# Kernel tuning notes

Measured on AMD Instinct MI355X. Metric: run time of the kernel, lower is better.

The kernel has to match this reference:

```python
import jax, jax.numpy as jnp
import numpy as np

B, S, D, H = 2, 2048, 1024, 16
DK = D // H

def setup_inputs() -> dict:
    key = jax.random.key(0)
    ks = jax.random.split(key, 11)
    scale = 1.0 / np.sqrt(D)
    inp = {
        'query': jax.random.normal(ks[0], (B, S, D), jnp.float32),
        'key':   jax.random.normal(ks[1], (B, S, D), jnp.float32),
        'value': jax.random.normal(ks[2], (B, S, D), jnp.float32),
        'wq': jax.random.normal(ks[3], (D, D), jnp.float32) * scale,
        'bq': jax.random.normal(ks[4], (D,), jnp.float32) * 0.01,
        'wk': jax.random.normal(ks[5], (D, D), jnp.float32) * scale,
        'bk': jax.random.normal(ks[6], (D,), jnp.float32) * 0.01,
        'wv': jax.random.normal(ks[7], (D, D), jnp.float32) * scale,
        'bv': jax.random.normal(ks[8], (D,), jnp.float32) * 0.01,
        'wo': jax.random.normal(ks[9], (D, D), jnp.float32) * scale,
        'bo': jax.random.normal(ks[10], (D,), jnp.float32) * 0.01,
    }
    return inp

def reference(query, key, value, wq, bq, wk, bk, wv, bv, wo, bo):
    nb = query.shape[0]
    # projections: torch nn.Linear computes x @ W^T + b; here weights stored as (in,out)
    def proj(x, w, b):
        return (x @ w + b).reshape(nb, -1, H, DK).transpose(0, 2, 1, 3)  # [B,H,S,dk]
    q = proj(query, wq, bq)
    k = proj(key, wk, bk)
    v = proj(value, wv, bv)
    scores = jnp.einsum('bhqd,bhkd->bhqk', q, k) / jnp.sqrt(jnp.float32(DK))
    p = jax.nn.softmax(scores, axis=-1)  # dropout p=0 (eval)
    x = jnp.einsum('bhqk,bhkd->bhqd', p, v)
    x = x.transpose(0, 2, 1, 3).reshape(nb, -1, H * DK)
    return x @ wo + bo
```

## Files before the change

kernel.cpp:

```cpp
#include <hip/hip_runtime.h>


typedef __attribute__((ext_vector_type(8))) __bf16 bf16x8;
typedef __attribute__((ext_vector_type(4))) __bf16 bf16x4;
typedef __attribute__((ext_vector_type(8))) float f32x8;
typedef __attribute__((ext_vector_type(4))) float f32x4;

#define MFMA16 __builtin_amdgcn_mfma_f32_16x16x32_bf16

union Bf8 { bf16x8 v; __bf16 e[8]; };

__device__ inline f32x4 zero4() { f32x4 z; z[0]=z[1]=z[2]=z[3]=0.f; return z; }

__device__ inline void load_lds16(const void* g, void* l) {
    __builtin_amdgcn_global_load_lds(
        (const __attribute__((address_space(1))) unsigned int*)g,
        (__attribute__((address_space(3))) unsigned int*)l, 16, 0, 0);
}

__global__ __launch_bounds__(256) void prep_all(
        const float* __restrict__ w0, const float* __restrict__ w1,
        const float* __restrict__ w2, const float* __restrict__ w3,
        const float* __restrict__ x0, const float* __restrict__ x1,
        const float* __restrict__ x2,
        __bf16* __restrict__ wt, __bf16* __restrict__ xb) {
    const int z = blockIdx.z;
    const int t = threadIdx.x;
    if (z < 4) {
        const float* src = z == 0 ? w0 : z == 1 ? w1 : z == 2 ? w2 : w3;
        __bf16* dst = wt + (size_t)z * 1048576;
        __shared__ float tile[32][33];
        const int tc = t & 31, tr = t >> 5;
        const int r0 = blockIdx.y * 32, c0 = blockIdx.x * 32;
#pragma unroll
        for (int i = 0; i < 4; i++) {
            int r = tr + i * 8;
            tile[r][tc] = src[(size_t)(r0 + r) * 1024 + c0 + tc];
        }
        __syncthreads();
#pragma unroll
        for (int i = 0; i < 4; i++) {
            int r = tr + i * 8;
            dst[(size_t)(c0 + r) * 1024 + r0 + tc] = (__bf16)tile[tc][r];
        }
    } else {
        const float* src = z == 4 ? x0 : z == 5 ? x1 : x2;
        __bf16* dst = xb + (size_t)(z - 4) * 4194304;
        int bid = blockIdx.y * 32 + blockIdx.x;
        size_t g = ((size_t)bid * 256 + t) * 16;
#pragma unroll
        for (int h = 0; h < 2; h++) {
            f32x8 a = *(const f32x8*)&src[g + h * 8];
            Bf8 tmp;
#pragma unroll
            for (int j = 0; j < 8; j++) tmp.e[j] = (__bf16)a[j];
            *(bf16x8*)&dst[g + h * 8] = tmp.v;
        }
    }
}

template <int MODE, typename OutT>
__device__ inline void gemm_fast_core(const __bf16* __restrict__ A,
                                      const __bf16* __restrict__ Bt,
                                      const float* __restrict__ bias,
                                      OutT* __restrict__ out, float scale) {
    __shared__ __bf16 As[8192];
    __shared__ __bf16 Bs[8192];
    const int t = threadIdx.x;
    const int wave = t >> 6, lane = t & 63, lm = lane & 15, quad = lane >> 4;
    const int m0 = blockIdx.y * 128, n0 = blockIdx.x * 128;
    const int wm = (wave >> 1) * 64, wn = (wave & 1) * 64;

    f32x4 acc[4][4];
#pragma unroll
    for (int i = 0; i < 4; i++)
#pragma unroll
        for (int j = 0; j < 4; j++) acc[i][j] = zero4();

    for (int k0 = 0; k0 < 1024; k0 += 64) {
#pragma unroll
        for (int i = 0; i < 4; i++) {
            int s = i * 256 + t;
            int row = s >> 3, cb = (s & 7) ^ (row & 7);
            size_t goff = (size_t)row * 1024 + k0 + cb * 8;
            __bf16* lbase = (__bf16*)((size_t)(i * 256 + wave * 64) * 8);
            load_lds16(&A[(size_t)m0 * 1024 + goff], &As[(size_t)(i * 256 + wave * 64) * 8]);
            load_lds16(&Bt[(size_t)n0 * 1024 + goff], &Bs[(size_t)(i * 256 + wave * 64) * 8]);
            (void)lbase;
        }
        __syncthreads();
#pragma unroll
        for (int ks = 0; ks < 2; ks++) {
            bf16x8 af[4], bfr[4];
#pragma unroll
            for (int mt = 0; mt < 4; mt++)
                af[mt] = *(const bf16x8*)&As[(wm + mt * 16 + lm) * 64 +
                                             (((ks * 4 + quad) ^ (lm & 7)) * 8)];
#pragma unroll
            for (int nt = 0; nt < 4; nt++)
                bfr[nt] = *(const bf16x8*)&Bs[(wn + nt * 16 + lm) * 64 +
                                              (((ks * 4 + quad) ^ (lm & 7)) * 8)];
#pragma unroll
            for (int mt = 0; mt < 4; mt++)
#pragma unroll
                for (int nt = 0; nt < 4; nt++)
                    acc[mt][nt] = MFMA16(af[mt], bfr[nt], acc[mt][nt], 0, 0, 0);
        }
        __syncthreads();
    }

    float bv4[4];
#pragma unroll
    for (int nt = 0; nt < 4; nt++) bv4[nt] = bias[n0 + wn + nt * 16 + lm];

#pragma unroll
    for (int mt = 0; mt < 4; mt++) {
#pragma unroll
        for (int r = 0; r < 4; r++) {
            int row = m0 + wm + mt * 16 + quad * 4 + r;
#pragma unroll
            for (int nt = 0; nt < 4; nt++) {
                int col = n0 + wn + nt * 16 + lm;
                float val = (acc[mt][nt][r] + bv4[nt]) * scale;
                size_t idx;
                if (MODE == 0) {
                    idx = (size_t)row * 1024 + col;
                } else {
                    int b = row >> 11, s = row & 2047, hh = col >> 6, dk = col & 63;
                    if (MODE == 1)
                        idx = (size_t)(b * 16 + hh) * 131072 + (size_t)s * 64 + dk;
                    else
                        idx = (size_t)(b * 16 + hh) * 131072 + (size_t)dk * 2048 + s;
                }
                out[idx] = (OutT)val;
            }
        }
    }
}

__global__ __launch_bounds__(256) void proj_fast(
        const __bf16* __restrict__ Xb, const __bf16* __restrict__ WT,
        const float* __restrict__ bq, const float* __restrict__ bk,
        const float* __restrict__ bv,
        __bf16* __restrict__ Q, __bf16* __restrict__ K, __bf16* __restrict__ Vt) {
    int z = blockIdx.z;
    if (z == 0)
        gemm_fast_core<1, __bf16>(Xb, WT, bq, Q, 0.125f);
    else if (z == 1)
        gemm_fast_core<1, __bf16>(Xb + 4194304, WT + 1048576, bk, K, 1.f);
    else
        gemm_fast_core<2, __bf16>(Xb + 8388608, WT + 2097152, bv, Vt, 1.f);
}

__global__ __launch_bounds__(256) void out_proj_fast(
        const __bf16* __restrict__ A, const __bf16* __restrict__ Bt,
        const float* __restrict__ bias, float* __restrict__ out) {
    gemm_fast_core<0, float>(A, Bt, bias, out, 1.f);
}

template <int MODE>
__device__ inline void gemm_core(const float* __restrict__ A,
                                 const __bf16* __restrict__ Bt,
                                 const float* __restrict__ bias,
                                 __bf16* __restrict__ out, float scale) {
    __shared__ __bf16 As[128 * 72];
    __shared__ __bf16 Bs[128 * 72];
    const int t = threadIdx.x;
    const int wave = t >> 6, lane = t & 63, lm = lane & 15, quad = lane >> 4;
    const int m0 = blockIdx.y * 128, n0 = blockIdx.x * 128;
    const int wm = (wave >> 1) * 64, wn = (wave & 1) * 64;

    f32x4 acc[4][4];
#pragma unroll
    for (int i = 0; i < 4; i++)
#pragma unroll
        for (int j = 0; j < 4; j++) acc[i][j] = zero4();

    for (int k0 = 0; k0 < 1024; k0 += 64) {
#pragma unroll
        for (int i = 0; i < 4; i++) {
            int c = i * 256 + t;
            int row = c >> 3, c8 = c & 7;
            size_t aoff = (size_t)(m0 + row) * 1024 + k0 + c8 * 8;
            f32x8 a = *(const f32x8*)&A[aoff];
            Bf8 tmp;
#pragma unroll
            for (int j = 0; j < 8; j++) tmp.e[j] = (__bf16)a[j];
            *(bf16x8*)&As[row * 72 + c8 * 8] = tmp.v;
            *(bf16x8*)&Bs[row * 72 + c8 * 8] =
                *(const bf16x8*)&Bt[(size_t)(n0 + row) * 1024 + k0 + c8 * 8];
        }
        __syncthreads();
#pragma unroll
        for (int ks = 0; ks < 2; ks++) {
            bf16x8 af[4], bfr[4];
#pragma unroll
            for (int mt = 0; mt < 4; mt++)
                af[mt] = *(const bf16x8*)&As[(wm + mt * 16 + lm) * 72 + ks * 32 + quad * 8];
#pragma unroll
            for (int nt = 0; nt < 4; nt++)
                bfr[nt] = *(const bf16x8*)&Bs[(wn + nt * 16 + lm) * 72 + ks * 32 + quad * 8];
#pragma unroll
            for (int mt = 0; mt < 4; mt++)
#pragma unroll
                for (int nt = 0; nt < 4; nt++)
                    acc[mt][nt] = MFMA16(af[mt], bfr[nt], acc[mt][nt], 0, 0, 0);
        }
        __syncthreads();
    }

    float bv4[4];
#pragma unroll
    for (int nt = 0; nt < 4; nt++) bv4[nt] = bias[n0 + wn + nt * 16 + lm];

#pragma unroll
    for (int mt = 0; mt < 4; mt++) {
#pragma unroll
        for (int r = 0; r < 4; r++) {
            int row = m0 + wm + mt * 16 + quad * 4 + r;
#pragma unroll
            for (int nt = 0; nt < 4; nt++) {
                int col = n0 + wn + nt * 16 + lm;
                float val = (acc[mt][nt][r] + bv4[nt]) * scale;
                size_t idx;
                int b = row >> 11, s = row & 2047, hh = col >> 6, dk = col & 63;
                if (MODE == 1)
                    idx = (size_t)(b * 16 + hh) * 131072 + (size_t)s * 64 + dk;
                else
                    idx = (size_t)(b * 16 + hh) * 131072 + (size_t)dk * 2048 + s;
                out[idx] = (__bf16)val;
            }
        }
    }
}

__global__ __launch_bounds__(256) void proj_slow(
        const float* __restrict__ q, const float* __restrict__ k,
        const float* __restrict__ v, const __bf16* __restrict__ WT,
        const float* __restrict__ bq, const float* __restrict__ bk,
        const float* __restrict__ bv,
        __bf16* __restrict__ Q, __bf16* __restrict__ K, __bf16* __restrict__ Vt) {
    int z = blockIdx.z;
    if (z == 0)      gemm_core<1>(q, WT,           bq, Q,  0.125f);
    else if (z == 1) gemm_core<1>(k, WT + 1048576, bk, K,  1.f);
    else             gemm_core<2>(v, WT + 2097152, bv, Vt, 1.f);
}

__global__ __launch_bounds__(256, 2) void attn_kernel(
        const __bf16* __restrict__ Q, const __bf16* __restrict__ K,
        const __bf16* __restrict__ Vt, __bf16* __restrict__ O) {
    __shared__ __bf16 Ks[8192];
    __shared__ __bf16 Vs[8192];
    __shared__ __bf16 Ps[4 * 32 * 136];
    const int t = threadIdx.x;
    const int wave = t >> 6, lane = t & 63, lm = lane & 15, quad = lane >> 4;
    const int q0 = blockIdx.x * 128;
    const int bh = blockIdx.y;
    const size_t base = (size_t)bh * 131072;

    bf16x8 bq[2][2];
    {
        int qrow = q0 + wave * 32;
#pragma unroll
        for (int nt = 0; nt < 2; nt++)
#pragma unroll
            for (int ks = 0; ks < 2; ks++)
                bq[nt][ks] = *(const bf16x8*)
                    &Q[base + (size_t)(qrow + nt * 16 + lm) * 64 + ks * 32 + quad * 8];
    }

    float m_run[2], l_run[2];
#pragma unroll
    for (int n = 0; n < 2; n++) { m_run[n] = -1e30f; l_run[n] = 0.f; }
    f32x4 o_acc[4][2];
#pragma unroll
    for (int mt = 0; mt < 4; mt++)
#pragma unroll
        for (int n = 0; n < 2; n++) o_acc[mt][n] = zero4();

    __bf16* Pw = &Ps[wave * 32 * 136];

    for (int kv0 = 0; kv0 < 2048; kv0 += 128) {
#pragma unroll
        for (int i = 0; i < 4; i++) {
            int s = i * 256 + t;
            {
                int row = s >> 3, cb = (s & 7) ^ (row & 7);
                load_lds16(&K[base + (size_t)(kv0 + row) * 64 + cb * 8],
                           &Ks[(size_t)(i * 256 + wave * 64) * 8]);
            }
            {
                int row = s >> 4, cb = (s & 15) ^ (row & 15);
                load_lds16(&Vt[base + (size_t)row * 2048 + kv0 + cb * 8],
                           &Vs[(size_t)(i * 256 + wave * 64) * 8]);
            }
        }
        __syncthreads();

        f32x4 sc[8][2];
#pragma unroll
        for (int mt = 0; mt < 8; mt++) {
            sc[mt][0] = zero4();
            sc[mt][1] = zero4();
#pragma unroll
            for (int ks = 0; ks < 2; ks++) {
                bf16x8 ak = *(const bf16x8*)&Ks[(mt * 16 + lm) * 64 +
                                                (((ks * 4 + quad) ^ (lm & 7)) * 8)];
                sc[mt][0] = MFMA16(ak, bq[0][ks], sc[mt][0], 0, 0, 0);
                sc[mt][1] = MFMA16(ak, bq[1][ks], sc[mt][1], 0, 0, 0);
            }
        }

#pragma unroll
        for (int nt = 0; nt < 2; nt++) {
            float mx = -1e30f;
#pragma unroll
            for (int mt = 0; mt < 8; mt++)
#pragma unroll
                for (int r = 0; r < 4; r++) mx = fmaxf(mx, sc[mt][nt][r]);
            mx = fmaxf(mx, __shfl_xor(mx, 16));
            mx = fmaxf(mx, __shfl_xor(mx, 32));
            float mn = fmaxf(m_run[nt], mx);
            float alpha = __expf(m_run[nt] - mn);
            m_run[nt] = mn;
            float su = 0.f;
#pragma unroll
            for (int mt = 0; mt < 8; mt++)
#pragma unroll
                for (int r = 0; r < 4; r++) {
                    float p = __expf(sc[mt][nt][r] - mn);
                    sc[mt][nt][r] = p;
                    su += p;
                }
            su += __shfl_xor(su, 16);
            su += __shfl_xor(su, 32);
            l_run[nt] = l_run[nt] * alpha + su;
#pragma unroll
            for (int mt = 0; mt < 4; mt++)
#pragma unroll
                for (int r = 0; r < 4; r++) o_acc[mt][nt][r] *= alpha;
        }

#pragma unroll
        for (int nt = 0; nt < 2; nt++)
#pragma unroll
            for (int mt = 0; mt < 8; mt++) {
                bf16x4 pk;
#pragma unroll
                for (int r = 0; r < 4; r++) pk[r] = (__bf16)sc[mt][nt][r];
                *(bf16x4*)&Pw[(nt * 16 + lm) * 136 + mt * 16 + quad * 4] = pk;
            }
        __asm__ volatile("" ::: "memory");

#pragma unroll
        for (int ks = 0; ks < 4; ks++) {
            bf16x8 bp[2];
#pragma unroll
            for (int nt = 0; nt < 2; nt++)
                bp[nt] = *(const bf16x8*)&Pw[(nt * 16 + lm) * 136 + ks * 32 + quad * 8];
#pragma unroll
            for (int mt = 0; mt < 4; mt++) {
                bf16x8 av = *(const bf16x8*)&Vs[(mt * 16 + lm) * 128 +
                                                (((ks * 4 + quad) ^ lm) * 8)];
                o_acc[mt][0] = MFMA16(av, bp[0], o_acc[mt][0], 0, 0, 0);
                o_acc[mt][1] = MFMA16(av, bp[1], o_acc[mt][1], 0, 0, 0);
            }
        }
        __syncthreads();
    }

#pragma unroll
    for (int nt = 0; nt < 2; nt++) {
        float inv = 1.f / l_run[nt];
#pragma unroll
        for (int mt = 0; mt < 4; mt++) {
            bf16x4 pk;
#pragma unroll
            for (int r = 0; r < 4; r++) pk[r] = (__bf16)(o_acc[mt][nt][r] * inv);
            *(bf16x4*)&Pw[(nt * 16 + lm) * 136 + mt * 16 + quad * 4] = pk;
        }
    }
    __asm__ volatile("" ::: "memory");
    {
        const int b = bh >> 4, h = bh & 15;
        int ql = lane >> 1, half = lane & 1;
        int srow = q0 + wave * 32 + ql;
#pragma unroll
        for (int j = 0; j < 4; j++) {
            bf16x8 v = *(const bf16x8*)&Pw[ql * 136 + half * 32 + j * 8];
            *(bf16x8*)&O[(size_t)(b * 2048 + srow) * 1024 + h * 64 + half * 32 + j * 8] = v;
        }
    }
}

extern "C" void kernel_launch(void* const* d_in, const int* in_sizes, int n_in,
                              void* d_out, int out_size, void* d_ws, size_t ws_size,
                              hipStream_t stream) {
    if (ws_size < ((size_t)40 << 20)) return;

    const float* query = (const float*)d_in[0];
    const float* key_  = (const float*)d_in[1];
    const float* value = (const float*)d_in[2];
    const float* wq = (const float*)d_in[3];
    const float* bq = (const float*)d_in[4];
    const float* wk = (const float*)d_in[5];
    const float* bk = (const float*)d_in[6];
    const float* wv = (const float*)d_in[7];
    const float* bv = (const float*)d_in[8];
    const float* wo = (const float*)d_in[9];
    const float* bo = (const float*)d_in[10];
    float* out = (float*)d_out;

    char* ws = (char*)d_ws;
    const bool big = ws_size >= ((size_t)56 << 20);
    __bf16* WT = (__bf16*)(ws);

    if (big) {
        __bf16* Xb  = (__bf16*)(ws + ((size_t)8 << 20));
        __bf16* Ow  = (__bf16*)(ws + ((size_t)8 << 20));
        __bf16* Qw  = (__bf16*)(ws + ((size_t)32 << 20));
        __bf16* Kw  = (__bf16*)(ws + ((size_t)40 << 20));
        __bf16* Vtw = (__bf16*)(ws + ((size_t)48 << 20));
        prep_all<<<dim3(32, 32, 7), dim3(256), 0, stream>>>(
            wq, wk, wv, wo, query, key_, value, WT, Xb);
        proj_fast<<<dim3(8, 32, 3), dim3(256), 0, stream>>>(
            Xb, WT, bq, bk, bv, Qw, Kw, Vtw);
        attn_kernel<<<dim3(16, 32), dim3(256), 0, stream>>>(Qw, Kw, Vtw, Ow);
        out_proj_fast<<<dim3(8, 32), dim3(256), 0, stream>>>(
            Ow, WT + 3 * 1048576, bo, out);
    } else {
        __bf16* Qw  = (__bf16*)(ws + ((size_t)8 << 20));
        __bf16* Kw  = (__bf16*)(ws + ((size_t)16 << 20));
        __bf16* Vtw = (__bf16*)(ws + ((size_t)24 << 20));
        __bf16* Ow  = (__bf16*)(ws + ((size_t)32 << 20));
        prep_all<<<dim3(32, 32, 4), dim3(256), 0, stream>>>(
            wq, wk, wv, wo, query, key_, value, WT, (__bf16*)nullptr);
        proj_slow<<<dim3(8, 32, 3), dim3(256), 0, stream>>>(
            query, key_, value, WT, bq, bk, bv, Qw, Kw, Vtw);
        attn_kernel<<<dim3(16, 32), dim3(256), 0, stream>>>(Qw, Kw, Vtw, Ow);
        out_proj_fast<<<dim3(8, 32), dim3(256), 0, stream>>>(
            Ow, WT + 3 * 1048576, bo, out);
    }
}
```

Baseline: 244.2 us.

## Use bf16 prep path in small workspace; LDS-stage transposed V stores; vectorize softmax

When the workspace is under 56 MB, query and value are now converted to bf16 and projected with the fast LDS-async GEMM. Key still goes through the slow fp32-input GEMM, with buffers reused to fit in 40 MB. The transposed V output is staged through swizzled shared memory, so each thread writes 16-byte vectors instead of scattered 2-byte stores. The softmax in the attention kernel is rewritten with f32x4 vector ops. Together these cut uncoalesced writes and fp32 loads, at the cost of an extra launch and a shared-memory round trip in the epilogue.

Result: slower. 250.0 us (+2.4%).

```diff
diff --git a/kernel.cpp b/kernel.cpp
--- a/kernel.cpp
+++ b/kernel.cpp
@@ -23,7 +23,8 @@
         const float* __restrict__ w2, const float* __restrict__ w3,
         const float* __restrict__ x0, const float* __restrict__ x1,
         const float* __restrict__ x2,
-        __bf16* __restrict__ wt, __bf16* __restrict__ xb) {
+        __bf16* __restrict__ wt, __bf16* __restrict__ d0,
+        __bf16* __restrict__ d1, __bf16* __restrict__ d2) {
     const int z = blockIdx.z;
     const int t = threadIdx.x;
     if (z < 4) {
@@ -45,7 +46,7 @@
         }
     } else {
         const float* src = z == 4 ? x0 : z == 5 ? x1 : x2;
-        __bf16* dst = xb + (size_t)(z - 4) * 4194304;
+        __bf16* dst = z == 4 ? d0 : z == 5 ? d1 : d2;
         int bid = blockIdx.y * 32 + blockIdx.x;
         size_t g = ((size_t)bid * 256 + t) * 16;
 #pragma unroll
@@ -64,8 +65,9 @@
                                       const __bf16* __restrict__ Bt,
                                       const float* __restrict__ bias,
                                       OutT* __restrict__ out, float scale) {
-    __shared__ __bf16 As[8192];
-    __shared__ __bf16 Bs[8192];
+    __shared__ __bf16 smem[16384];
+    __bf16* As = smem;
+    __bf16* Bs = smem + 8192;
     const int t = threadIdx.x;
     const int wave = t >> 6, lane = t & 63, lm = lane & 15, quad = lane >> 4;
     const int m0 = blockIdx.y * 128, n0 = blockIdx.x * 128;
@@ -83,10 +85,10 @@
             int s = i * 256 + t;
             int row = s >> 3, cb = (s & 7) ^ (row & 7);
             size_t goff = (size_t)row * 1024 + k0 + cb * 8;
-            __bf16* lbase = (__bf16*)((size_t)(i * 256 + wave * 64) * 8);
-            load_lds16(&A[(size_t)m0 * 1024 + goff], &As[(size_t)(i * 256 + wave * 64) * 8]);
-            load_lds16(&Bt[(size_t)n0 * 1024 + goff], &Bs[(size_t)(i * 256 + wave * 64) * 8]);
-            (void)lbase;
+            load_lds16(&A[(size_t)m0 * 1024 + goff],
+                       &As[(size_t)(i * 256 + wave * 64) * 8]);
+            load_lds16(&Bt[(size_t)n0 * 1024 + goff],
+                       &Bs[(size_t)(i * 256 + wave * 64) * 8]);
         }
         __syncthreads();
 #pragma unroll
@@ -113,32 +115,56 @@
 #pragma unroll
     for (int nt = 0; nt < 4; nt++) bv4[nt] = bias[n0 + wn + nt * 16 + lm];
 
-#pragma unroll
-    for (int mt = 0; mt < 4; mt++) {
-#pragma unroll
-        for (int r = 0; r < 4; r++) {
-            int row = m0 + wm + mt * 16 + quad * 4 + r;
-#pragma unroll
-            for (int nt = 0; nt < 4; nt++) {
-                int col = n0 + wn + nt * 16 + lm;
-                float val = (acc[mt][nt][r] + bv4[nt]) * scale;
-                size_t idx;
-                if (MODE == 0) {
-                    idx = (size_t)row * 1024 + col;
-                } else {
-                    int b = row >> 11, s = row & 2047, hh = col >> 6, dk = col & 63;
-                    if (MODE == 1)
+    if (MODE == 2) {
+#pragma unroll
+        for (int mt = 0; mt < 4; mt++)
+#pragma unroll
+            for (int r = 0; r < 4; r++) {
+                int rr = wm + mt * 16 + quad * 4 + r;
+#pragma unroll
+                for (int nt = 0; nt < 4; nt++) {
+                    int c = wn + nt * 16 + lm;
+                    smem[c * 128 + (rr ^ (8 * (c & 15)))] =
+                        (__bf16)((acc[mt][nt][r] + bv4[nt]) * scale);
+                }
+            }
+        __syncthreads();
+        const int b = m0 >> 11;
+#pragma unroll
+        for (int it = 0; it < 8; it++) {
+            int g = it * 256 + t;
+            int c = g >> 4, gr = g & 15;
+            bf16x8 v = *(const bf16x8*)&smem[c * 128 + ((gr * 8) ^ (8 * (c & 15)))];
+            int col = n0 + c, hh = col >> 6, dk = col & 63;
+            int sglob = (m0 & 2047) + gr * 8;
+            size_t idx = (size_t)(b * 16 + hh) * 131072 + (size_t)dk * 2048 + sglob;
+            *(bf16x8*)&out[idx] = v;
+        }
+    } else {
+#pragma unroll
+        for (int mt = 0; mt < 4; mt++) {
+#pragma unroll
+            for (int r = 0; r < 4; r++) {
+                int row = m0 + wm + mt * 16 + quad * 4 + r;
+#pragma unroll
+                for (int nt = 0; nt < 4; nt++) {
+                    int col = n0 + wn + nt * 16 + lm;
+                    float val = (acc[mt][nt][r] + bv4[nt]) * scale;
+                    size_t idx;
+                    if (MODE == 0) {
+                        idx = (size_t)row * 1024 + col;
+                    } else {
+                        int b = row >> 11, s = row & 2047, hh = col >> 6, dk = col & 63;
                         idx = (size_t)(b * 16 + hh) * 131072 + (size_t)s * 64 + dk;
-                    else
-                        idx = (size_t)(b * 16 + hh) * 131072 + (size_t)dk * 2048 + s;
+                    }
+                    out[idx] = (OutT)val;
                 }
-                out[idx] = (OutT)val;
-            }
-        }
-    }
-}
-
-__global__ __launch_bounds__(256) void proj_fast(
+            }
+        }
+    }
+}
+
+__global__ __launch_bounds__(256) void proj_fast3(
         const __bf16* __restrict__ Xb, const __bf16* __restrict__ WT,
         const float* __restrict__ bq, const float* __restrict__ bk,
         const float* __restrict__ bv,
@@ -152,17 +178,26 @@
         gemm_fast_core<2, __bf16>(Xb + 8388608, WT + 2097152, bv, Vt, 1.f);
 }
 
+__global__ __launch_bounds__(256) void proj_qv(
+        const __bf16* __restrict__ Xq, const __bf16* __restrict__ Xv,
+        const __bf16* __restrict__ WT,
+        const float* __restrict__ bq, const float* __restrict__ bv,
+        __bf16* __restrict__ Q, __bf16* __restrict__ Vt) {
+    if (blockIdx.z == 0)
+        gemm_fast_core<1, __bf16>(Xq, WT, bq, Q, 0.125f);
+    else
+        gemm_fast_core<2, __bf16>(Xv, WT + 2097152, bv, Vt, 1.f);
+}
+
 __global__ __launch_bounds__(256) void out_proj_fast(
         const __bf16* __restrict__ A, const __bf16* __restrict__ Bt,
         const float* __restrict__ bias, float* __restrict__ out) {
     gemm_fast_core<0, float>(A, Bt, bias, out, 1.f);
 }
 
-template <int MODE>
-__device__ inline void gemm_core(const float* __restrict__ A,
-                                 const __bf16* __restrict__ Bt,
-                                 const float* __restrict__ bias,
-                                 __bf16* __restrict__ out, float scale) {
+__global__ __launch_bounds__(256) void proj_k_slow(
+        const float* __restrict__ A, const __bf16* __restrict__ Bt,
+        const float* __restrict__ bias, __bf16* __restrict__ out) {
     __shared__ __bf16 As[128 * 72];
     __shared__ __bf16 Bs[128 * 72];
     const int t = threadIdx.x;
@@ -181,8 +216,7 @@
         for (int i = 0; i < 4; i++) {
             int c = i * 256 + t;
             int row = c >> 3, c8 = c & 7;
-            size_t aoff = (size_t)(m0 + row) * 1024 + k0 + c8 * 8;
-            f32x8 a = *(const f32x8*)&A[aoff];
+            f32x8 a = *(const f32x8*)&A[(size_t)(m0 + row) * 1024 + k0 + c8 * 8];
             Bf8 tmp;
 #pragma unroll
             for (int j = 0; j < 8; j++) tmp.e[j] = (__bf16)a[j];
@@ -214,36 +248,18 @@
     for (int nt = 0; nt < 4; nt++) bv4[nt] = bias[n0 + wn + nt * 16 + lm];
 
 #pragma unroll
-    for (int mt = 0; mt < 4; mt++) {
+    for (int mt = 0; mt < 4; mt++)
 #pragma unroll
         for (int r = 0; r < 4; r++) {
             int row = m0 + wm + mt * 16 + quad * 4 + r;
 #pragma unroll
             for (int nt = 0; nt < 4; nt++) {
                 int col = n0 + wn + nt * 16 + lm;
-                float val = (acc[mt][nt][r] + bv4[nt]) * scale;
-                size_t idx;
+                float val = acc[mt][nt][r] + bv4[nt];
                 int b = row >> 11, s = row & 2047, hh = col >> 6, dk = col & 63;
-                if (MODE == 1)
-                    idx = (size_t)(b * 16 + hh) * 131072 + (size_t)s * 64 + dk;
-                else
-                    idx = (size_t)(b * 16 + hh) * 131072 + (size_t)dk * 2048 + s;
-                out[idx] = (__bf16)val;
-            }
-        }
-    }
-}
-
-__global__ __launch_bounds__(256) void proj_slow(
-        const float* __restrict__ q, const float* __restrict__ k,
-        const float* __restrict__ v, const __bf16* __restrict__ WT,
-        const float* __restrict__ bq, const float* __restrict__ bk,
-        const float* __restrict__ bv,
-        __bf16* __restrict__ Q, __bf16* __restrict__ K, __bf16* __restrict__ Vt) {
-    int z = blockIdx.z;
-    if (z == 0)      gemm_core<1>(q, WT,           bq, Q,  0.125f);
-    else if (z == 1) gemm_core<1>(k, WT + 1048576, bk, K,  1.f);
-    else             gemm_core<2>(v, WT + 2097152, bv, Vt, 1.f);
+                out[(size_t)(b * 16 + hh) * 131072 + (size_t)s * 64 + dk] = (__bf16)val;
+            }
+        }
 }
 
 __global__ __launch_bounds__(256, 2) void attn_kernel(
@@ -316,29 +332,30 @@
             float mx = -1e30f;
 #pragma unroll
             for (int mt = 0; mt < 8; mt++)
-#pragma unroll
-                for (int r = 0; r < 4; r++) mx = fmaxf(mx, sc[mt][nt][r]);
+                mx = fmaxf(mx, fmaxf(fmaxf(sc[mt][nt][0], sc[mt][nt][1]),
+                                     fmaxf(sc[mt][nt][2], sc[mt][nt][3])));
             mx = fmaxf(mx, __shfl_xor(mx, 16));
             mx = fmaxf(mx, __shfl_xor(mx, 32));
             float mn = fmaxf(m_run[nt], mx);
             float alpha = __expf(m_run[nt] - mn);
             m_run[nt] = mn;
-            float su = 0.f;
-#pragma unroll
-            for (int mt = 0; mt < 8; mt++)
-#pragma unroll
-                for (int r = 0; r < 4; r++) {
-                    float p = __expf(sc[mt][nt][r] - mn);
-                    sc[mt][nt][r] = p;
-                    su += p;
-                }
+            f32x4 mn4; mn4[0] = mn4[1] = mn4[2] = mn4[3] = mn;
+            f32x4 su4 = zero4();
+#pragma unroll
+            for (int mt = 0; mt < 8; mt++) {
+                f32x4 p = sc[mt][nt] - mn4;
+#pragma unroll
+                for (int r = 0; r < 4; r++) p[r] = __expf(p[r]);
+                sc[mt][nt] = p;
+                su4 += p;
+            }
+            float su = (su4[0] + su4[1]) + (su4[2] + su4[3]);
             su += __shfl_xor(su, 16);
             su += __shfl_xor(su, 32);
             l_run[nt] = l_run[nt] * alpha + su;
-#pragma unroll
-            for (int mt = 0; mt < 4; mt++)
-#pragma unroll
-                for (int r = 0; r < 4; r++) o_acc[mt][nt][r] *= alpha;
+            f32x4 a4; a4[0] = a4[1] = a4[2] = a4[3] = alpha;
+#pragma unroll
+            for (int mt = 0; mt < 4; mt++) o_acc[mt][nt] *= a4;
         }
 
 #pragma unroll
@@ -412,33 +429,36 @@
     float* out = (float*)d_out;
 
     char* ws = (char*)d_ws;
-    const bool big = ws_size >= ((size_t)56 << 20);
     __bf16* WT = (__bf16*)(ws);
 
-    if (big) {
+    if (ws_size >= ((size_t)56 << 20)) {
         __bf16* Xb  = (__bf16*)(ws + ((size_t)8 << 20));
         __bf16* Ow  = (__bf16*)(ws + ((size_t)8 << 20));
         __bf16* Qw  = (__bf16*)(ws + ((size_t)32 << 20));
         __bf16* Kw  = (__bf16*)(ws + ((size_t)40 << 20));
         __bf16* Vtw = (__bf16*)(ws + ((size_t)48 << 20));
         prep_all<<<dim3(32, 32, 7), dim3(256), 0, stream>>>(
-            wq, wk, wv, wo, query, key_, value, WT, Xb);
-        proj_fast<<<dim3(8, 32, 3), dim3(256), 0, stream>>>(
+            wq, wk, wv, wo, query, key_, value, WT,
+            Xb, Xb + 4194304, Xb + 8388608);
+        proj_fast3<<<dim3(8, 32, 3), dim3(256), 0, stream>>>(
             Xb, WT, bq, bk, bv, Qw, Kw, Vtw);
         attn_kernel<<<dim3(16, 32), dim3(256), 0, stream>>>(Qw, Kw, Vtw, Ow);
         out_proj_fast<<<dim3(8, 32), dim3(256), 0, stream>>>(
             Ow, WT + 3 * 1048576, bo, out);
     } else {
-        __bf16* Qw  = (__bf16*)(ws + ((size_t)8 << 20));
-        __bf16* Kw  = (__bf16*)(ws + ((size_t)16 << 20));
-        __bf16* Vtw = (__bf16*)(ws + ((size_t)24 << 20));
-        __bf16* Ow  = (__bf16*)(ws + ((size_t)32 << 20));
-        prep_all<<<dim3(32, 32, 4), dim3(256), 0, stream>>>(
-            wq, wk, wv, wo, query, key_, value, WT, (__bf16*)nullptr);
-        proj_slow<<<dim3(8, 32, 3), dim3(256), 0, stream>>>(
-            query, key_, value, WT, bq, bk, bv, Qw, Kw, Vtw);
-        attn_kernel<<<dim3(16, 32), dim3(256), 0, stream>>>(Qw, Kw, Vtw, Ow);
+        __bf16* R1 = (__bf16*)(ws + ((size_t)8  << 20));
+        __bf16* R2 = (__bf16*)(ws + ((size_t)16 << 20));
+        __bf16* R3 = (__bf16*)(ws + ((size_t)24 << 20));
+        __bf16* R4 = (__bf16*)(ws + ((size_t)32 << 20));
+        prep_all<<<dim3(32, 32, 6), dim3(256), 0, stream>>>(
+            wq, wk, wv, wo, query, value, (const float*)nullptr, WT,
+            R1, R2, (__bf16*)nullptr);
+        proj_qv<<<dim3(8, 32, 2), dim3(256), 0, stream>>>(
+            R1, R2, WT, bq, bv, R3, R4);
+        proj_k_slow<<<dim3(8, 32), dim3(256), 0, stream>>>(
+            key_, WT + 1048576, bk, R1);
+        attn_kernel<<<dim3(16, 32), dim3(256), 0, stream>>>(R3, R1, R4, R2);
         out_proj_fast<<<dim3(8, 32), dim3(256), 0, stream>>>(
-            Ow, WT + 3 * 1048576, bo, out);
-    }
-}
+            R2, WT + 3 * 1048576, bo, out);
+    }
+}
```
